# Performance work log

Hardware: AMD Instinct MI355X
Metric: run time of the kernel (lower is better)

## Reference

```python
import jax, jax.numpy as jnp
import numpy as np

EPS = 1e-5
SLOPE = 0.2
K = 20
BINS = [1, 2, 4, 8, 16, 32]


def knn(x_t, k):
    # x_t: (B, N, C) -> idx (B, N, k) of nearest neighbors (by L2, incl. self)
    xx = jnp.sum(x_t * x_t, axis=-1)  # (B, N)
    pd = 2.0 * jnp.einsum('bnc,bmc->bnm', x_t, x_t) - xx[:, :, None] - xx[:, None, :]
    _, idx = jax.lax.top_k(pd, k)
    return idx


def edge_features(x_t, idx):
    # x_t: (B, N, C), idx: (B, N, k) -> (B, N, k, 2C) = [nbr - ctr, ctr]
    B = x_t.shape[0]
    nbr = x_t[jnp.arange(B)[:, None, None], idx]          # (B, N, k, C) gather
    ctr = jnp.broadcast_to(x_t[:, :, None, :], nbr.shape)
    return jnp.concatenate([nbr - ctr, ctr], axis=-1)


def batchnorm(h, gamma, beta, axes):
    # training-mode BN: normalize with batch statistics over `axes` (channel last)
    m = jnp.mean(h, axis=axes, keepdims=True)
    v = jnp.var(h, axis=axes, keepdims=True)
    return (h - m) * jax.lax.rsqrt(v + EPS) * gamma + beta


def lrelu(h):
    return jnp.where(h >= 0, h, SLOPE * h)


def edgeconv(x_t, W, g, b):
    # 1x1 conv over edge features + BN + LeakyReLU + max over k neighbors
    e = edge_features(x_t, knn(x_t, K))            # (B, N, k, 2C)
    h = jnp.einsum('bnkc,oc->bnko', e, W)          # per-edge GEMM
    h = lrelu(batchnorm(h, g, b, (0, 1, 2)))
    return jnp.max(h, axis=2)                      # (B, N, Cout)


def setup_inputs() -> dict:
    key = jax.random.key(0)
    ks = jax.random.split(key, 8)
    B, N = 4, 2048
    d = {'x': jax.random.normal(ks[0], (B, 3, N), dtype=jnp.float32)}
    # conv weights (out, in); BN gamma=1, beta=0 as in torch init
    d['W1'] = jax.random.normal(ks[1], (64, 6), dtype=jnp.float32) * 0.1
    d['g1'] = jnp.ones((64,), jnp.float32); d['b1'] = jnp.zeros((64,), jnp.float32)
    d['W2'] = jax.random.normal(ks[2], (64, 128), dtype=jnp.float32) * 0.1
    d['g2'] = jnp.ones((64,), jnp.float32); d['b2'] = jnp.zeros((64,), jnp.float32)
    d['W3'] = jax.random.normal(ks[3], (128, 128), dtype=jnp.float32) * 0.1
    d['g3'] = jnp.ones((128,), jnp.float32); d['b3'] = jnp.zeros((128,), jnp.float32)
    d['W4'] = jax.random.normal(ks[4], (256, 256), dtype=jnp.float32) * 0.1
    d['g4'] = jnp.ones((256,), jnp.float32); d['b4'] = jnp.zeros((256,), jnp.float32)
    d['W5'] = jax.random.normal(ks[5], (1024, 512), dtype=jnp.float32) * 0.05
    d['g5'] = jnp.ones((1024,), jnp.float32); d['b5'] = jnp.zeros((1024,), jnp.float32)
    d['Wf'] = jax.random.normal(ks[6], (256, 1024), dtype=jnp.float32) * 0.03
    d['bfeat'] = jax.random.normal(ks[7], (256,), dtype=jnp.float32) * 0.01
    return d


def reference(x, W1, g1, b1, W2, g2, b2, W3, g3, b3, W4, g4, b4, W5, g5, b5, Wf, bfeat):
    B, _, N = x.shape
    x_t = jnp.transpose(x, (0, 2, 1))              # (B, N, 3)
    x1 = edgeconv(x_t, W1, g1, b1)                 # (B, N, 64)
    x2 = edgeconv(x1, W2, g2, b2)                  # (B, N, 64)
    x3 = edgeconv(x2, W3, g3, b3)                  # (B, N, 128)
    x4 = edgeconv(x3, W4, g4, b4)                  # (B, N, 256)
    xc = jnp.concatenate([x1, x2, x3, x4], axis=-1)  # (B, N, 512)
    h = jnp.einsum('bnc,oc->bno', xc, W5)          # (B, N, 1024)
    h = lrelu(batchnorm(h, g5, b5, (0, 1)))
    F = h.shape[-1]
    feats = []
    for nb in BINS:  # horizontal pyramid pooling over contiguous point chunks
        z = h.reshape(B, nb, N // nb, F)
        feats.append(jnp.max(z, axis=2) + jnp.mean(z, axis=2))
    bins = jnp.concatenate(feats, axis=1)          # (B, 63, F)
    out = jnp.einsum('bsf,of->sbo', bins, Wf) + bfeat  # (63, B, 256)
    return out
```

## Files before the change

kernel.cpp:

```cpp
#include <hip/hip_runtime.h>
#include <hip/hip_bf16.h>
#include <cstdint>
#include <cstddef>

#define B_SZ   4
#define N_PTS  2048
#define KNN    20
#define BN_ROWS (B_SZ * N_PTS)
#define EPSV   1e-5f
#define SLOPEV 0.2f

typedef __attribute__((ext_vector_type(8))) short bf16x8;
typedef __attribute__((ext_vector_type(4))) float f32x4;

__global__ void k_transpose(const float* __restrict__ x, float* __restrict__ xt,
                            float* __restrict__ xx)
{
    int i = blockIdx.x * 256 + threadIdx.x;
    if (i >= BN_ROWS) return;
    int b = i >> 11, n = i & 2047;
    float v0 = x[((b * 3 + 0) << 11) + n];
    float v1 = x[((b * 3 + 1) << 11) + n];
    float v2 = x[((b * 3 + 2) << 11) + n];
    xt[i * 3 + 0] = v0; xt[i * 3 + 1] = v1; xt[i * 3 + 2] = v2;
    xx[i] = fmaf(v0, v0, fmaf(v1, v1, v2 * v2));
}

__global__ void k_prepw_all(const float* __restrict__ W1, const float* __restrict__ W2,
                            const float* __restrict__ W3, const float* __restrict__ W4,
                            const float* __restrict__ W5, const float* __restrict__ Wf,
                            float* __restrict__ wc, __hip_bfloat16* __restrict__ w5h,
                            float* __restrict__ wft)
{
    int i = blockIdx.x * 256 + threadIdx.x;
    if (i >= 876928) return;
    if (i >= 614784) {
        int e = i - 614784;
        int o = e >> 10, f = e & 1023;
        wft[f * 256 + o] = Wf[e];
        return;
    }
    if (i >= 90496) {
        int e = i - 90496;
        w5h[e] = __float2bfloat16(W5[e]);
        return;
    }
    const float* W; int O, C, off;
    if      (i < 384)   { W = W1; O = 64;  C = 3;   off = 0; }
    else if (i < 8576)  { W = W2; O = 64;  C = 64;  off = 384; }
    else if (i < 24960) { W = W3; O = 128; C = 64;  off = 8576; }
    else                { W = W4; O = 256; C = 128; off = 24960; }
    int e = i - off, j = e / C, c = e - j * C;
    float v;
    if (j < O) v = W[j * 2 * C + c];
    else { int jo = j - O; v = W[jo * 2 * C + C + c] - W[jo * 2 * C + c]; }
    wc[i] = v;
}

template<bool VEC>
__launch_bounds__(512)
__global__ void k_dist(const float* __restrict__ A, int lda,
                       const float* __restrict__ xx,
                       float* __restrict__ C1, int Kd)
{
    constexpr int LDA_ = 132;
    constexpr int LDT_ = 68;
    __shared__ float smem[8704];
    float* As = smem;
    float* Bs = smem + 32 * LDA_;
    float* T  = smem;
    const int tid = threadIdx.x;
    const int tx  = tid & 31;
    const int ty  = tid >> 5;

    int t = blockIdx.x;
    int it, jt;
    if (t < 120) {
        int i = 0;
        for (; i < 15; ++i) { int cnt = 15 - i; if (t < cnt) break; t -= cnt; }
        it = i; jt = i + 1 + t;
    } else {
        it = jt = t - 120;
    }
    const int m0 = it * 128;
    const int n0 = jt * 128;
    const int b  = blockIdx.z;
    const float* Ab = A + (size_t)b * N_PTS * lda;

    float acc[2][4][4] = {};

    for (int k0 = 0; k0 < Kd; k0 += 32) {
        #pragma unroll
        for (int r = 0; r < 2; ++r) {
            int e = r * 512 + tid, row = e >> 3, kq = e & 7;
            if constexpr (VEC) {
                float4 v = *(const float4*)&Ab[(size_t)(m0 + row) * lda + k0 + kq * 4];
                As[(kq * 4 + 0) * LDA_ + row] = v.x;
                As[(kq * 4 + 1) * LDA_ + row] = v.y;
                As[(kq * 4 + 2) * LDA_ + row] = v.z;
                As[(kq * 4 + 3) * LDA_ + row] = v.w;
            } else {
                #pragma unroll
                for (int j = 0; j < 4; ++j) {
                    int kg = k0 + kq * 4 + j;
                    As[(kq * 4 + j) * LDA_ + row] =
                        (kg < Kd) ? Ab[(size_t)(m0 + row) * lda + kg] : 0.f;
                }
            }
        }
        #pragma unroll
        for (int r = 0; r < 2; ++r) {
            int e = r * 512 + tid, row = e >> 3, kq = e & 7;
            if constexpr (VEC) {
                float4 v = *(const float4*)&Ab[(size_t)(n0 + row) * lda + k0 + kq * 4];
                Bs[(kq * 4 + 0) * LDA_ + row] = v.x;
                Bs[(kq * 4 + 1) * LDA_ + row] = v.y;
                Bs[(kq * 4 + 2) * LDA_ + row] = v.z;
                Bs[(kq * 4 + 3) * LDA_ + row] = v.w;
            } else {
                #pragma unroll
                for (int j = 0; j < 4; ++j) {
                    int kg = k0 + kq * 4 + j;
                    Bs[(kq * 4 + j) * LDA_ + row] =
                        (kg < Kd) ? Ab[(size_t)(n0 + row) * lda + kg] : 0.f;
                }
            }
        }
        __syncthreads();

        if constexpr (VEC) {
            float4 ca0 = *(const float4*)&As[ty * 4];
            float4 ca1 = *(const float4*)&As[64 + ty * 4];
            float4 cb  = *(const float4*)&Bs[tx * 4];
            #pragma unroll
            for (int kk = 0; kk < 32; ++kk) {
                float4 na0, na1, nb;
                if (kk < 31) {
                    na0 = *(const float4*)&As[(kk + 1) * LDA_ + ty * 4];
                    na1 = *(const float4*)&As[(kk + 1) * LDA_ + 64 + ty * 4];
                    nb  = *(const float4*)&Bs[(kk + 1) * LDA_ + tx * 4];
                }
                float av[2][4] = {{ca0.x,ca0.y,ca0.z,ca0.w},{ca1.x,ca1.y,ca1.z,ca1.w}};
                float bw[4] = {cb.x, cb.y, cb.z, cb.w};
                #pragma unroll
                for (int ih = 0; ih < 2; ++ih)
                    #pragma unroll
                    for (int ii = 0; ii < 4; ++ii)
                        #pragma unroll
                        for (int jj = 0; jj < 4; ++jj)
                            acc[ih][ii][jj] = fmaf(av[ih][ii], bw[jj], acc[ih][ii][jj]);
                if (kk < 31) { ca0 = na0; ca1 = na1; cb = nb; }
            }
        } else {
            int klen = Kd - k0; if (klen > 32) klen = 32;
            #pragma unroll 8
            for (int kk = 0; kk < klen; ++kk) {
                float4 a0 = *(const float4*)&As[kk * LDA_ + ty * 4];
                float4 a1 = *(const float4*)&As[kk * LDA_ + 64 + ty * 4];
                float4 bq = *(const float4*)&Bs[kk * LDA_ + tx * 4];
                float av[2][4] = {{a0.x,a0.y,a0.z,a0.w},{a1.x,a1.y,a1.z,a1.w}};
                float bw[4] = {bq.x, bq.y, bq.z, bq.w};
                #pragma unroll
                for (int ih = 0; ih < 2; ++ih)
                    #pragma unroll
                    for (int ii = 0; ii < 4; ++ii)
                        #pragma unroll
                        for (int jj = 0; jj < 4; ++jj)
                            acc[ih][ii][jj] = fmaf(av[ih][ii], bw[jj], acc[ih][ii][jj]);
            }
        }
        __syncthreads();
    }

    const float* xxb = xx + b * N_PTS;
    float xj[4];
    {
        float4 v = *(const float4*)&xxb[n0 + tx * 4];
        xj[0] = v.x; xj[1] = v.y; xj[2] = v.z; xj[3] = v.w;
    }
    float xiv[2][4];
    #pragma unroll
    for (int ih = 0; ih < 2; ++ih)
        #pragma unroll
        for (int i = 0; i < 4; ++i)
            xiv[ih][i] = xxb[m0 + ih * 64 + ty * 4 + i];
    const bool diag = (m0 == n0);
    const size_t zoff = (size_t)b * N_PTS;

    #pragma unroll
    for (int ih = 0; ih < 2; ++ih)
        #pragma unroll
        for (int i = 0; i < 4; ++i) {
            int gi = m0 + ih * 64 + ty * 4 + i;
            float xi = xiv[ih][i];
            int gj = n0 + tx * 4;
            float4 v;
            v.x = 2.f * acc[ih][i][0] - xi - xj[0];
            v.y = 2.f * acc[ih][i][1] - xi - xj[1];
            v.z = 2.f * acc[ih][i][2] - xi - xj[2];
            v.w = 2.f * acc[ih][i][3] - xi - xj[3];
            if (diag) {
                if (gi == gj + 0) v.x = 0.f;
                if (gi == gj + 1) v.y = 0.f;
                if (gi == gj + 2) v.z = 0.f;
                if (gi == gj + 3) v.w = 0.f;
            }
            *(float4*)&C1[(zoff + gi) * N_PTS + gj] = v;
        }

    if (!diag) {
        #pragma unroll
        for (int ih = 0; ih < 2; ++ih) {
            #pragma unroll
            for (int c = 0; c < 4; ++c) {
                float xjc = xj[c];
                float4 tv;
                tv.x = 2.f * acc[ih][0][c] - xjc - xiv[ih][0];
                tv.y = 2.f * acc[ih][1][c] - xjc - xiv[ih][1];
                tv.z = 2.f * acc[ih][2][c] - xjc - xiv[ih][2];
                tv.w = 2.f * acc[ih][3][c] - xjc - xiv[ih][3];
                *(float4*)&T[(tx * 4 + c) * LDT_ + ty * 4] = tv;
            }
            __syncthreads();
            #pragma unroll
            for (int r = 0; r < 4; ++r) {
                int e = r * 512 + tid;
                int jr = e >> 4, c4 = e & 15;
                float4 tv = *(const float4*)&T[jr * LDT_ + c4 * 4];
                *(float4*)&C1[(zoff + n0 + jr) * N_PTS + m0 + ih * 64 + c4 * 4] = tv;
            }
            __syncthreads();
        }
    }
}

__launch_bounds__(256)
__global__ void k_gemm5(const unsigned short* __restrict__ Ah,
                        const unsigned short* __restrict__ Bh,
                        float* __restrict__ Cf,
                        float* __restrict__ ssum, float* __restrict__ ssumsq)
{
    constexpr int LDA = 72;
    __shared__ unsigned short As[128 * LDA];
    __shared__ unsigned short Bs[128 * LDA];
    const int tid  = threadIdx.x;
    const int lane = tid & 63;
    const int w    = tid >> 6;
    const int wr   = w >> 1, wcl = w & 1;
    const int quad = lane >> 4;
    const int l16  = lane & 15;
    const int m0 = blockIdx.y * 128;
    const int n0 = blockIdx.x * 128;

    f32x4 acc[4][4] = {};

    for (int k0 = 0; k0 < 512; k0 += 64) {
        #pragma unroll
        for (int r = 0; r < 4; ++r) {
            int e = r * 256 + tid, row = e >> 3, kq = e & 7;
            *(uint4*)&As[row * LDA + kq * 8] =
                *(const uint4*)&Ah[(size_t)(m0 + row) * 512 + k0 + kq * 8];
        }
        #pragma unroll
        for (int r = 0; r < 4; ++r) {
            int e = r * 256 + tid, row = e >> 3, kq = e & 7;
            *(uint4*)&Bs[row * LDA + kq * 8] =
                *(const uint4*)&Bh[(size_t)(n0 + row) * 512 + k0 + kq * 8];
        }
        __syncthreads();
        #pragma unroll
        for (int kk = 0; kk < 64; kk += 32) {
            bf16x8 af[4], bfr[4];
            #pragma unroll
            for (int i = 0; i < 4; ++i)
                af[i] = *(const bf16x8*)&As[(wr * 64 + i * 16 + l16) * LDA + kk + quad * 8];
            #pragma unroll
            for (int j = 0; j < 4; ++j)
                bfr[j] = *(const bf16x8*)&Bs[(wcl * 64 + j * 16 + l16) * LDA + kk + quad * 8];
            #pragma unroll
            for (int i = 0; i < 4; ++i)
                #pragma unroll
                for (int j = 0; j < 4; ++j)
                    acc[i][j] = __builtin_amdgcn_mfma_f32_16x16x32_bf16(af[i], bfr[j], acc[i][j], 0, 0, 0);
        }
        __syncthreads();
    }

    #pragma unroll
    for (int i = 0; i < 4; ++i) {
        int rbase = m0 + wr * 64 + i * 16 + quad * 4;
        #pragma unroll
        for (int j = 0; j < 4; ++j) {
            int col = n0 + wcl * 64 + j * 16 + l16;
            #pragma unroll
            for (int r = 0; r < 4; ++r)
                Cf[(size_t)(rbase + r) * 1024 + col] = acc[i][j][r];
        }
    }

    float* sredS = (float*)As;
    float* sredQ = (float*)Bs;
    #pragma unroll
    for (int j = 0; j < 4; ++j) {
        float s = 0.f, q = 0.f;
        #pragma unroll
        for (int i = 0; i < 4; ++i)
            #pragma unroll
            for (int r = 0; r < 4; ++r) {
                float v = acc[i][j][r];
                s += v; q = fmaf(v, v, q);
            }
        int coll = wcl * 64 + j * 16 + l16;
        int slot = wr * 4 + quad;
        sredS[coll * 8 + slot] = s;
        sredQ[coll * 8 + slot] = q;
    }
    __syncthreads();
    if (tid < 128) {
        float s = 0.f, q = 0.f;
        #pragma unroll
        for (int t = 0; t < 8; ++t) { s += sredS[tid * 8 + t]; q += sredQ[tid * 8 + t]; }
        ssum  [blockIdx.y * 1024 + n0 + tid] = s;
        ssumsq[blockIdx.y * 1024 + n0 + tid] = q;
    }
}

template<bool VEC>
__launch_bounds__(256)
__global__ void k_selgd(const float* __restrict__ D2, int* __restrict__ idx_out,
                        const float* __restrict__ A, int lda,
                        const float* __restrict__ Bm, int ldb,
                        float* __restrict__ C1, float* __restrict__ C2,
                        int Nn, int Kd, int gdBlocks, int gdsh)
{
    constexpr int LDA_ = 132;
    constexpr int LDB_ = 68;
    __shared__ float smem[32 * LDA_ + 32 * LDB_];

    if ((int)blockIdx.x < gdBlocks) {
        float* As = smem;
        float* Bs = smem + 32 * LDA_;
        const int tid = threadIdx.x;
        const int tx  = tid & 15;
        const int ty  = tid >> 4;
        const int gdx = Nn >> 6;
        const int bx  = blockIdx.x & (gdx - 1);
        const int by  = blockIdx.x >> gdsh;
        const int m0 = by * 128;
        const int n0 = bx * 64;

        float acc[2][4][4] = {};

        for (int k0 = 0; k0 < Kd; k0 += 32) {
            #pragma unroll
            for (int r = 0; r < 4; ++r) {
                int e = r * 256 + tid, row = e >> 3, kq = e & 7;
                if constexpr (VEC) {
                    float4 v = *(const float4*)&A[(size_t)(m0 + row) * lda + k0 + kq * 4];
                    As[(kq * 4 + 0) * LDA_ + row] = v.x;
                    As[(kq * 4 + 1) * LDA_ + row] = v.y;
                    As[(kq * 4 + 2) * LDA_ + row] = v.z;
                    As[(kq * 4 + 3) * LDA_ + row] = v.w;
                } else {
                    #pragma unroll
                    for (int j = 0; j < 4; ++j) {
                        int kg = k0 + kq * 4 + j;
                        As[(kq * 4 + j) * LDA_ + row] =
                            (kg < Kd) ? A[(size_t)(m0 + row) * lda + kg] : 0.f;
                    }
                }
            }
            #pragma unroll
            for (int r = 0; r < 2; ++r) {
                int e = r * 256 + tid, row = e >> 3, kq = e & 7;
                if constexpr (VEC) {
                    float4 v = *(const float4*)&Bm[(size_t)(n0 + row) * ldb + k0 + kq * 4];
                    Bs[(kq * 4 + 0) * LDB_ + row] = v.x;
                    Bs[(kq * 4 + 1) * LDB_ + row] = v.y;
                    Bs[(kq * 4 + 2) * LDB_ + row] = v.z;
                    Bs[(kq * 4 + 3) * LDB_ + row] = v.w;
                } else {
                    #pragma unroll
                    for (int j = 0; j < 4; ++j) {
                        int kg = k0 + kq * 4 + j;
                        Bs[(kq * 4 + j) * LDB_ + row] =
                            (kg < Kd) ? Bm[(size_t)(n0 + row) * ldb + kg] : 0.f;
                    }
                }
            }
            __syncthreads();

            if constexpr (VEC) {
                float4 ca0 = *(const float4*)&As[ty * 4];
                float4 ca1 = *(const float4*)&As[64 + ty * 4];
                float4 cb0 = *(const float4*)&Bs[tx * 4];
                #pragma unroll
                for (int kk = 0; kk < 32; ++kk) {
                    float4 na0, na1, nb0;
                    if (kk < 31) {
                        na0 = *(const float4*)&As[(kk + 1) * LDA_ + ty * 4];
                        na1 = *(const float4*)&As[(kk + 1) * LDA_ + 64 + ty * 4];
                        nb0 = *(const float4*)&Bs[(kk + 1) * LDB_ + tx * 4];
                    }
                    float av[2][4] = {{ca0.x,ca0.y,ca0.z,ca0.w},{ca1.x,ca1.y,ca1.z,ca1.w}};
                    float bw[4] = {cb0.x, cb0.y, cb0.z, cb0.w};
                    #pragma unroll
                    for (int ih = 0; ih < 2; ++ih)
                        #pragma unroll
                        for (int ii = 0; ii < 4; ++ii)
                            #pragma unroll
                            for (int jj = 0; jj < 4; ++jj)
                                acc[ih][ii][jj] = fmaf(av[ih][ii], bw[jj], acc[ih][ii][jj]);
                    if (kk < 31) { ca0 = na0; ca1 = na1; cb0 = nb0; }
                }
            } else {
                int klen = Kd - k0; if (klen > 32) klen = 32;
                #pragma unroll 8
                for (int kk = 0; kk < klen; ++kk) {
                    float4 a0 = *(const float4*)&As[kk * LDA_ + ty * 4];
                    float4 a1 = *(const float4*)&As[kk * LDA_ + 64 + ty * 4];
                    float4 bq = *(const float4*)&Bs[kk * LDB_ + tx * 4];
                    float av[2][4] = {{a0.x,a0.y,a0.z,a0.w},{a1.x,a1.y,a1.z,a1.w}};
                    float bw[4] = {bq.x, bq.y, bq.z, bq.w};
                    #pragma unroll
                    for (int ih = 0; ih < 2; ++ih)
                        #pragma unroll
                        for (int ii = 0; ii < 4; ++ii)
                            #pragma unroll
                            for (int jj = 0; jj < 4; ++jj)
                                acc[ih][ii][jj] = fmaf(av[ih][ii], bw[jj], acc[ih][ii][jj]);
                }
            }
            __syncthreads();
        }

        const int Oo = Nn >> 1;
        #pragma unroll
        for (int ih = 0; ih < 2; ++ih)
            #pragma unroll
            for (int i = 0; i < 4; ++i) {
                int row = m0 + ih * 64 + ty * 4 + i;
                int colg = n0 + tx * 4;
                float4 v = make_float4(acc[ih][i][0], acc[ih][i][1],
                                       acc[ih][i][2], acc[ih][i][3]);
                if (colg < Oo) *(float4*)&C1[(size_t)row * Oo + colg] = v;
                else           *(float4*)&C2[(size_t)row * Oo + colg - Oo] = v;
            }
        return;
    }

    const int lane = threadIdx.x & 63;
    const int w    = threadIdx.x >> 6;
    const int qloc = ((int)blockIdx.x - gdBlocks) * 4 + w;
    const float* row = D2 + (size_t)qloc * N_PTS;

    unsigned key[32];
    #pragma unroll
    for (int c = 0; c < 8; ++c) {
        float4 v = *(const float4*)&row[c * 256 + lane * 4];
        float vv[4] = {v.x, v.y, v.z, v.w};
        #pragma unroll
        for (int r = 0; r < 4; ++r) {
            unsigned u = __float_as_uint(vv[r]);
            key[c * 4 + r] = ((int)u >= 0) ? (u | 0x80000000u) : ~u;
        }
    }

    unsigned lmax = 0u;
    #pragma unroll
    for (int e = 0; e < 32; ++e) lmax = (key[e] > lmax) ? key[e] : lmax;
    unsigned gmin = lmax, gmax = lmax;
    #pragma unroll
    for (int s = 32; s >= 1; s >>= 1) {
        unsigned o1 = __shfl_xor(gmin, s, 64);
        unsigned o2 = __shfl_xor(gmax, s, 64);
        gmin = (o1 < gmin) ? o1 : gmin;
        gmax = (o2 > gmax) ? o2 : gmax;
    }

    unsigned lo = gmin, hi2 = gmax;
    while (lo < hi2) {
        unsigned mid = lo + ((hi2 - lo) >> 1);
        int c = __popcll(__ballot(lmax > mid));
        if (c < KNN) hi2 = mid; else lo = mid + 1;
    }
    unsigned hi = gmax;

    unsigned c0 = 0u, c1 = 0u, c2 = 0u, c3 = 0u;
    int nc = 0;
    #pragma unroll
    for (int e = 0; e < 32; ++e) {
        unsigned k = key[e];
        if (k >= lo) {
            if (nc == 0) c0 = k; else if (nc == 1) c1 = k;
            else if (nc == 2) c2 = k; else if (nc == 3) c3 = k;
            ++nc;
        }
    }
    if (__ballot(nc > 4)) {
        while (lo < hi) {
            unsigned mid = lo + ((hi - lo) >> 1);
            int cnt = 0;
            #pragma unroll
            for (int e = 0; e < 32; ++e)
                cnt += __popcll(__ballot(key[e] > mid));
            if (cnt < KNN) hi = mid; else lo = mid + 1;
        }
    } else {
        while (lo < hi) {
            unsigned mid = lo + ((hi - lo) >> 1);
            int cnt = __popcll(__ballot(c0 > mid))
                    + __popcll(__ballot(c1 > mid))
                    + __popcll(__ballot(c2 > mid))
                    + __popcll(__ballot(c3 > mid));
            if (cnt < KNN) hi = mid; else lo = mid + 1;
        }
    }
    const unsigned T = lo;

    int* outp = idx_out + (size_t)qloc * KNN;
    const unsigned long long ltmask = (lane == 0) ? 0ull : (~0ull >> (64 - lane));
    int base = 0;
    #pragma unroll
    for (int e = 0; e < 32; ++e) {
        bool p = key[e] > T;
        unsigned long long m = __ballot(p);
        if (p) {
            int pos = base + __popcll(m & ltmask);
            outp[pos] = (e >> 2) * 256 + lane * 4 + (e & 3);
        }
        base += __popcll(m);
    }
    #pragma unroll
    for (int e = 0; e < 32; ++e) {
        bool p = key[e] == T;
        unsigned long long m = __ballot(p);
        if (p) {
            int pos = base + __popcll(m & ltmask);
            if (pos < KNN) outp[pos] = (e >> 2) * 256 + lane * 4 + (e & 3);
        }
        base += __popcll(m);
    }
}

template<int O, int NSEQ>
__launch_bounds__(256)
__global__ void k_gather(const float* __restrict__ gtab, const float* __restrict__ dtab,
                         const int* __restrict__ idx, const float* __restrict__ gamma,
                         float* __restrict__ hsel,
                         float* __restrict__ ssum, float* __restrict__ ssumsq)
{
    constexpr int NPB = 256 / O;
    const int grp = threadIdx.x / O;
    const int o   = threadIdx.x & (O - 1);
    const float g = gamma[o];
    float accS = 0.f, accS2 = 0.f;
    const int rowsPerBlock = NPB * NSEQ;
    const int batch = blockIdx.x & 3;
    const int chunk = blockIdx.x >> 2;
    const int bbase = batch << 11;
    for (int s = 0; s < NSEQ; ++s) {
        int row = bbase + chunk * rowsPerBlock + s * NPB + grp;
        const int* ip = idx + (size_t)row * KNN;
        float gmax = -INFINITY, gmin = INFINITY, gs = 0.f, gs2 = 0.f;
        for (int k = 0; k < KNN; ++k) {
            int nb = ip[k];
            float v = gtab[(size_t)(bbase + nb) * O + o];
            gmax = fmaxf(gmax, v);
            gmin = fminf(gmin, v);
            gs  += v;
            gs2  = fmaf(v, v, gs2);
        }
        float d = dtab[(size_t)row * O + o];
        float keep = (g >= 0.f) ? gmax : gmin;
        hsel[(size_t)row * O + o] = keep + d;
        accS  += gs + (float)KNN * d;
        accS2 += gs2 + 2.f * d * gs + (float)KNN * d * d;
    }
    int bank = blockIdx.x & 63;
    atomicAdd(&ssum[bank * O + o], accS);
    atomicAdd(&ssumsq[bank * O + o], accS2);
}

template<int O, bool WRITE_XX>
__launch_bounds__(256)
__global__ void k_normalize(const float* __restrict__ hsel,
                            const float* __restrict__ ssum, const float* __restrict__ ssumsq,
                            const float* __restrict__ gamma, const float* __restrict__ beta,
                            float invM, float* __restrict__ xcs,
                            __hip_bfloat16* __restrict__ xch, float* __restrict__ xx)
{
    const int tid = threadIdx.x;
    const int o   = tid & (O - 1);
    float s = 0.f, s2 = 0.f;
    #pragma unroll 8
    for (int bk = 0; bk < 64; ++bk) { s += ssum[bk * O + o]; s2 += ssumsq[bk * O + o]; }
    float mean = s * invM;
    float var  = fmaf(-mean, mean, s2 * invM);
    float sc   = gamma[o] * rsqrtf(var + EPSV);
    float sh   = beta[o] - mean * sc;

    constexpr int R = 256 / O;
    const int rloc = tid / O;
    __shared__ float part[4];
    const int ngroups = BN_ROWS / R;
    for (int gidx = blockIdx.x; gidx < ngroups; gidx += gridDim.x) {
        int row = gidx * R + rloc;
        size_t i = (size_t)row * O + o;
        float h = hsel[i];
        float y = fmaf(h, sc, sh);
        y = (y >= 0.f) ? y : SLOPEV * y;
        xcs[(size_t)row * 512 + o] = y;
        xch[(size_t)row * 512 + o] = __float2bfloat16(y);
        if constexpr (WRITE_XX) {
            float p = y * y;
            #pragma unroll
            for (int sft = 32; sft >= 1; sft >>= 1) p += __shfl_xor(p, sft, 64);
            if constexpr (O == 64) {
                if ((tid & 63) == 0) xx[row] = p;
            } else {
                if ((tid & 63) == 0) part[tid >> 6] = p;
                __syncthreads();
                if constexpr (O == 128) {
                    if (tid < 2) xx[gidx * R + tid] = part[2 * tid] + part[2 * tid + 1];
                } else {
                    if (tid == 0) xx[gidx * R] = (part[0] + part[1]) + (part[2] + part[3]);
                }
                __syncthreads();
            }
        }
    }
}

__global__ void k_seg(const float* __restrict__ h,
                      const float* __restrict__ ssum, const float* __restrict__ ssumsq,
                      const float* __restrict__ gamma, const float* __restrict__ beta,
                      float* __restrict__ smax, float* __restrict__ ssumseg)
{
    int f = blockIdx.y * 256 + threadIdx.x;
    float s = 0.f, s2 = 0.f;
    #pragma unroll 8
    for (int bk = 0; bk < 64; ++bk) { s += ssum[bk * 1024 + f]; s2 += ssumsq[bk * 1024 + f]; }
    const float invM = 1.f / (float)BN_ROWS;
    float mean = s * invM;
    float var  = fmaf(-mean, mean, s2 * invM);
    float sc   = gamma[f] * rsqrtf(var + EPSV);
    float sh   = beta[f] - mean * sc;

    int seg = blockIdx.x;
    float mx = -INFINITY, sm = 0.f;
    int n0 = seg * 64;
    for (int i = 0; i < 64; ++i) {
        float v = fmaf(h[(size_t)(n0 + i) * 1024 + f], sc, sh);
        v = (v >= 0.f) ? v : SLOPEV * v;
        mx = fmaxf(mx, v); sm += v;
    }
    smax[(size_t)seg * 1024 + f]    = mx;
    ssumseg[(size_t)seg * 1024 + f] = sm;
}

__launch_bounds__(256)
__global__ void k_final(const float* __restrict__ smax, const float* __restrict__ ssg,
                        const float* __restrict__ Wft, const float* __restrict__ bfeat,
                        float* __restrict__ out)
{
    __shared__ float row[1024];
    __shared__ float part[1024];
    const int tid = threadIdx.x;
    int sb = blockIdx.x;
    int s = sb >> 2, b = sb & 3;
    int nb = (s == 0) ? 1 : (s < 3) ? 2 : (s < 7) ? 4 : (s < 15) ? 8 : (s < 31) ? 16 : 32;
    int idxL = s - (nb - 1);
    int segc = 32 / nb;
    int seg0 = b * 32 + idxL * segc;
    float inv = 1.f / (float)(64 * segc);
    for (int c = tid; c < 1024; c += 256) {
        float mx = -INFINITY, sm = 0.f;
        for (int t = 0; t < segc; ++t) {
            mx = fmaxf(mx, smax[(size_t)(seg0 + t) * 1024 + c]);
            sm += ssg[(size_t)(seg0 + t) * 1024 + c];
        }
        row[c] = mx + sm * inv;
    }
    __syncthreads();

    const int lane = tid & 63;
    const int w    = tid >> 6;
    const float* rw = row + w * 256;
    const float* wp = Wft + (size_t)(w * 256) * 256 + lane * 4;
    float4 a0 = {0,0,0,0}, a1 = {0,0,0,0}, a2 = {0,0,0,0}, a3 = {0,0,0,0};
    for (int f = 0; f < 256; f += 4) {
        float r0 = rw[f + 0], r1 = rw[f + 1], r2 = rw[f + 2], r3 = rw[f + 3];
        float4 w0 = *(const float4*)&wp[(size_t)(f + 0) * 256];
        float4 w1 = *(const float4*)&wp[(size_t)(f + 1) * 256];
        float4 w2 = *(const float4*)&wp[(size_t)(f + 2) * 256];
        float4 w3 = *(const float4*)&wp[(size_t)(f + 3) * 256];
        a0.x = fmaf(r0, w0.x, a0.x); a0.y = fmaf(r0, w0.y, a0.y);
        a0.z = fmaf(r0, w0.z, a0.z); a0.w = fmaf(r0, w0.w, a0.w);
        a1.x = fmaf(r1, w1.x, a1.x); a1.y = fmaf(r1, w1.y, a1.y);
        a1.z = fmaf(r1, w1.z, a1.z); a1.w = fmaf(r1, w1.w, a1.w);
        a2.x = fmaf(r2, w2.x, a2.x); a2.y = fmaf(r2, w2.y, a2.y);
        a2.z = fmaf(r2, w2.z, a2.z); a2.w = fmaf(r2, w2.w, a2.w);
        a3.x = fmaf(r3, w3.x, a3.x); a3.y = fmaf(r3, w3.y, a3.y);
        a3.z = fmaf(r3, w3.z, a3.z); a3.w = fmaf(r3, w3.w, a3.w);
    }
    float4 a;
    a.x = (a0.x + a1.x) + (a2.x + a3.x);
    a.y = (a0.y + a1.y) + (a2.y + a3.y);
    a.z = (a0.z + a1.z) + (a2.z + a3.z);
    a.w = (a0.w + a1.w) + (a2.w + a3.w);
    *(float4*)&part[w * 256 + lane * 4] = a;
    __syncthreads();
    int o = tid;
    float acc = (part[o] + part[256 + o]) + (part[512 + o] + part[768 + o]);
    out[(size_t)sb * 256 + o] = acc + bfeat[o];
}

extern "C" void kernel_launch(void* const* d_in, const int* in_sizes, int n_in,
                              void* d_out, int out_size, void* d_ws, size_t ws_size,
                              hipStream_t stream)
{
    const float* x  = (const float*)d_in[0];
    const float* W1 = (const float*)d_in[1];
    const float* g1 = (const float*)d_in[2];
    const float* b1 = (const float*)d_in[3];
    const float* W2 = (const float*)d_in[4];
    const float* g2 = (const float*)d_in[5];
    const float* b2 = (const float*)d_in[6];
    const float* W3 = (const float*)d_in[7];
    const float* g3 = (const float*)d_in[8];
    const float* b3 = (const float*)d_in[9];
    const float* W4 = (const float*)d_in[10];
    const float* g4 = (const float*)d_in[11];
    const float* b4 = (const float*)d_in[12];
    const float* W5 = (const float*)d_in[13];
    const float* g5 = (const float*)d_in[14];
    const float* b5 = (const float*)d_in[15];
    const float* Wf = (const float*)d_in[16];
    const float* bfeat = (const float*)d_in[17];
    float* out = (float*)d_out;
    float* ws  = (float*)d_ws;

    float* xt1   = ws + 0;
    int*   idx   = (int*)(ws + 24576);
    float* xx    = ws + 188416;
    float* xc    = ws + 196608;
    float* hsel  = ws + 4390912;
    float* stats = ws + 8585216;
    float* smax  = ws + 8650752;
    float* ssg   = ws + 8781824;
    float* wc    = ws + 8912896;
    float* big   = ws + 9003520;
    __hip_bfloat16* xch = (__hip_bfloat16*)(ws + 25780736);
    __hip_bfloat16* w5h = (__hip_bfloat16*)(ws + 27877888);
    float* wft   = ws + 28140032;
    float* l5s   = ws + 28402176;
    float* l5q   = ws + 28467712;
    float* gtab  = ws + 28533248;
    float* dtab  = ws + 30630400;

    hipMemsetAsync(stats, 0, 65536 * sizeof(float), stream);
    k_transpose<<<32, 256, 0, stream>>>(x, xt1, xx);
    k_prepw_all<<<3426, 256, 0, stream>>>(W1, W2, W3, W4, W5, Wf, wc, w5h, wft);

    const float invMk = 1.f / (float)(BN_ROWS * KNN);

    {
        float* ss = stats + 0;
        k_dist<false><<<dim3(136, 1, 4), 512, 0, stream>>>(xt1, 3, xx, big, 3);
        k_selgd<false><<<128 + 2048, 256, 0, stream>>>(big, idx, xt1, 3, wc, 3, gtab, dtab, 128, 3, 128, 1);
        k_gather<64, 8><<<256, 256, 0, stream>>>(gtab, dtab, idx, g1, hsel, ss, ss + 4096);
        k_normalize<64, true><<<512, 256, 0, stream>>>(hsel, ss, ss + 4096, g1, b1, invMk, xc + 0, xch + 0, xx);
    }
    {
        float* ss = stats + 8192;
        k_dist<true><<<dim3(136, 1, 4), 512, 0, stream>>>(xc + 0, 512, xx, big, 64);
        k_selgd<true><<<128 + 2048, 256, 0, stream>>>(big, idx, xc + 0, 512, wc + 384, 64, gtab, dtab, 128, 64, 128, 1);
        k_gather<64, 8><<<256, 256, 0, stream>>>(gtab, dtab, idx, g2, hsel, ss, ss + 4096);
        k_normalize<64, true><<<512, 256, 0, stream>>>(hsel, ss, ss + 4096, g2, b2, invMk, xc + 64, xch + 64, xx);
    }
    {
        float* ss = stats + 16384;
        k_dist<true><<<dim3(136, 1, 4), 512, 0, stream>>>(xc + 64, 512, xx, big, 64);
        k_selgd<true><<<256 + 2048, 256, 0, stream>>>(big, idx, xc + 64, 512, wc + 8576, 64, gtab, dtab, 256, 64, 256, 2);
        k_gather<128, 8><<<512, 256, 0, stream>>>(gtab, dtab, idx, g3, hsel, ss, ss + 8192);
        k_normalize<128, true><<<512, 256, 0, stream>>>(hsel, ss, ss + 8192, g3, b3, invMk, xc + 128, xch + 128, xx);
    }
    {
        float* ss = stats + 32768;
        k_dist<true><<<dim3(136, 1, 4), 512, 0, stream>>>(xc + 128, 512, xx, big, 128);
        k_selgd<true><<<512 + 2048, 256, 0, stream>>>(big, idx, xc + 128, 512, wc + 24960, 128, gtab, dtab, 512, 128, 512, 3);
        k_gather<256, 8><<<1024, 256, 0, stream>>>(gtab, dtab, idx, g4, hsel, ss, ss + 16384);
        k_normalize<256, false><<<512, 256, 0, stream>>>(hsel, ss, ss + 16384, g4, b4, invMk, xc + 256, xch + 256, xx);
    }
    {
        k_gemm5<<<dim3(8, 64), 256, 0, stream>>>((const unsigned short*)xch, (const unsigned short*)w5h, big, l5s, l5q);
        k_seg<<<dim3(128, 4), 256, 0, stream>>>(big, l5s, l5q, g5, b5, smax, ssg);
        k_final<<<252, 256, 0, stream>>>(smax, ssg, wft, bfeat, out);
    }
}
```

Measured before the change: 488.2 us.

## Double-buffer shared-memory tiles in vectorized pairwise-distance GEMM kernel

Restructures the VEC path of the k_dist distance GEMM to use two shared-memory stages. The global loads for the next K-slice are issued into registers before the current slice's FMA loop and stored into the alternate buffer afterwards, so each step needs one barrier instead of two. Shared memory per block roughly doubles (about 34 KB to about 68 KB), which may reduce occupancy. The non-vectorized path is unchanged apart from being split out.

```diff
diff --git a/kernel.cpp b/kernel.cpp
--- a/kernel.cpp
+++ b/kernel.cpp
@@ -65,9 +65,8 @@
 {
     constexpr int LDA_ = 132;
     constexpr int LDT_ = 68;
-    __shared__ float smem[8704];
-    float* As = smem;
-    float* Bs = smem + 32 * LDA_;
+    constexpr int BUFF = 32 * LDA_ * 2;
+    __shared__ float smem[2 * BUFF];
     float* T  = smem;
     const int tid = threadIdx.x;
     const int tx  = tid & 31;
@@ -89,56 +88,67 @@
 
     float acc[2][4][4] = {};
 
-    for (int k0 = 0; k0 < Kd; k0 += 32) {
-        #pragma unroll
-        for (int r = 0; r < 2; ++r) {
-            int e = r * 512 + tid, row = e >> 3, kq = e & 7;
-            if constexpr (VEC) {
-                float4 v = *(const float4*)&Ab[(size_t)(m0 + row) * lda + k0 + kq * 4];
-                As[(kq * 4 + 0) * LDA_ + row] = v.x;
-                As[(kq * 4 + 1) * LDA_ + row] = v.y;
-                As[(kq * 4 + 2) * LDA_ + row] = v.z;
-                As[(kq * 4 + 3) * LDA_ + row] = v.w;
-            } else {
-                #pragma unroll
-                for (int j = 0; j < 4; ++j) {
-                    int kg = k0 + kq * 4 + j;
-                    As[(kq * 4 + j) * LDA_ + row] =
-                        (kg < Kd) ? Ab[(size_t)(m0 + row) * lda + kg] : 0.f;
-                }
-            }
-        }
-        #pragma unroll
-        for (int r = 0; r < 2; ++r) {
-            int e = r * 512 + tid, row = e >> 3, kq = e & 7;
-            if constexpr (VEC) {
-                float4 v = *(const float4*)&Ab[(size_t)(n0 + row) * lda + k0 + kq * 4];
-                Bs[(kq * 4 + 0) * LDA_ + row] = v.x;
-                Bs[(kq * 4 + 1) * LDA_ + row] = v.y;
-                Bs[(kq * 4 + 2) * LDA_ + row] = v.z;
-                Bs[(kq * 4 + 3) * LDA_ + row] = v.w;
-            } else {
-                #pragma unroll
-                for (int j = 0; j < 4; ++j) {
-                    int kg = k0 + kq * 4 + j;
-                    Bs[(kq * 4 + j) * LDA_ + row] =
-                        (kg < Kd) ? Ab[(size_t)(n0 + row) * lda + kg] : 0.f;
-                }
-            }
-        }
+    if constexpr (VEC) {
+        const int nst  = Kd >> 5;
+        const int row0 = tid >> 3, kq0 = tid & 7;
+        const float* gA0 = Ab + (size_t)(m0 + row0) * lda + kq0 * 4;
+        const float* gA1 = Ab + (size_t)(m0 + row0 + 64) * lda + kq0 * 4;
+        const float* gB0 = Ab + (size_t)(n0 + row0) * lda + kq0 * 4;
+        const float* gB1 = Ab + (size_t)(n0 + row0 + 64) * lda + kq0 * 4;
+        const int s0 = (kq0 * 4) * LDA_ + row0;
+
+        float4 pA0, pA1, pB0, pB1;
+
+#define KD_STORE_TILE(BASEPTR) do {                                  \
+        float* As_m = (BASEPTR);                                     \
+        float* Bs_m = (BASEPTR) + 32 * LDA_;                         \
+        As_m[s0 + 0 * LDA_]      = pA0.x;                            \
+        As_m[s0 + 1 * LDA_]      = pA0.y;                            \
+        As_m[s0 + 2 * LDA_]      = pA0.z;                            \
+        As_m[s0 + 3 * LDA_]      = pA0.w;                            \
+        As_m[s0 + 0 * LDA_ + 64] = pA1.x;                            \
+        As_m[s0 + 1 * LDA_ + 64] = pA1.y;                            \
+        As_m[s0 + 2 * LDA_ + 64] = pA1.z;                            \
+        As_m[s0 + 3 * LDA_ + 64] = pA1.w;                            \
+        Bs_m[s0 + 0 * LDA_]      = pB0.x;                            \
+        Bs_m[s0 + 1 * LDA_]      = pB0.y;                            \
+        Bs_m[s0 + 2 * LDA_]      = pB0.z;                            \
+        Bs_m[s0 + 3 * LDA_]      = pB0.w;                            \
+        Bs_m[s0 + 0 * LDA_ + 64] = pB1.x;                            \
+        Bs_m[s0 + 1 * LDA_ + 64] = pB1.y;                            \
+        Bs_m[s0 + 2 * LDA_ + 64] = pB1.z;                            \
+        Bs_m[s0 + 3 * LDA_ + 64] = pB1.w;                            \
+    } while (0)
+
+        pA0 = *(const float4*)(gA0);
+        pA1 = *(const float4*)(gA1);
+        pB0 = *(const float4*)(gB0);
+        pB1 = *(const float4*)(gB1);
+        KD_STORE_TILE(smem);
         __syncthreads();
 
-        if constexpr (VEC) {
-            float4 ca0 = *(const float4*)&As[ty * 4];
-            float4 ca1 = *(const float4*)&As[64 + ty * 4];
-            float4 cb  = *(const float4*)&Bs[tx * 4];
+        for (int step = 0; step < nst; ++step) {
+            float* As_ = smem + (step & 1) * BUFF;
+            float* Bs_ = As_ + 32 * LDA_;
+            const bool more = (step + 1 < nst);
+            if (more) {
+                const int ko = (step + 1) << 5;
+                pA0 = *(const float4*)(gA0 + ko);
+                pA1 = *(const float4*)(gA1 + ko);
+                pB0 = *(const float4*)(gB0 + ko);
+                pB1 = *(const float4*)(gB1 + ko);
+            }
+
+            float4 ca0 = *(const float4*)&As_[ty * 4];
+            float4 ca1 = *(const float4*)&As_[64 + ty * 4];
+            float4 cb  = *(const float4*)&Bs_[tx * 4];
             #pragma unroll
             for (int kk = 0; kk < 32; ++kk) {
                 float4 na0, na1, nb;
                 if (kk < 31) {
-                    na0 = *(const float4*)&As[(kk + 1) * LDA_ + ty * 4];
-                    na1 = *(const float4*)&As[(kk + 1) * LDA_ + 64 + ty * 4];
-                    nb  = *(const float4*)&Bs[(kk + 1) * LDA_ + tx * 4];
+                    na0 = *(const float4*)&As_[(kk + 1) * LDA_ + ty * 4];
+                    na1 = *(const float4*)&As_[(kk + 1) * LDA_ + 64 + ty * 4];
+                    nb  = *(const float4*)&Bs_[(kk + 1) * LDA_ + tx * 4];
                 }
                 float av[2][4] = {{ca0.x,ca0.y,ca0.z,ca0.w},{ca1.x,ca1.y,ca1.z,ca1.w}};
                 float bw[4] = {cb.x, cb.y, cb.z, cb.w};
@@ -151,7 +161,36 @@
                             acc[ih][ii][jj] = fmaf(av[ih][ii], bw[jj], acc[ih][ii][jj]);
                 if (kk < 31) { ca0 = na0; ca1 = na1; cb = nb; }
             }
-        } else {
+            if (more) KD_STORE_TILE(smem + ((step + 1) & 1) * BUFF);
+            __syncthreads();
+        }
+#undef KD_STORE_TILE
+    } else {
+        float* As = smem;
+        float* Bs = smem + 32 * LDA_;
+        for (int k0 = 0; k0 < Kd; k0 += 32) {
+            #pragma unroll
+            for (int r = 0; r < 2; ++r) {
+                int e = r * 512 + tid, row = e >> 3, kq = e & 7;
+                #pragma unroll
+                for (int j = 0; j < 4; ++j) {
+                    int kg = k0 + kq * 4 + j;
+                    As[(kq * 4 + j) * LDA_ + row] =
+                        (kg < Kd) ? Ab[(size_t)(m0 + row) * lda + kg] : 0.f;
+                }
+            }
+            #pragma unroll
+            for (int r = 0; r < 2; ++r) {
+                int e = r * 512 + tid, row = e >> 3, kq = e & 7;
+                #pragma unroll
+                for (int j = 0; j < 4; ++j) {
+                    int kg = k0 + kq * 4 + j;
+                    Bs[(kq * 4 + j) * LDA_ + row] =
+                        (kg < Kd) ? Ab[(size_t)(n0 + row) * lda + kg] : 0.f;
+                }
+            }
+            __syncthreads();
+
             int klen = Kd - k0; if (klen > 32) klen = 32;
             #pragma unroll 8
             for (int kk = 0; kk < klen; ++kk) {
@@ -168,8 +207,8 @@
                         for (int jj = 0; jj < 4; ++jj)
                             acc[ih][ii][jj] = fmaf(av[ih][ii], bw[jj], acc[ih][ii][jj]);
             }
-        }
-        __syncthreads();
+            __syncthreads();
+        }
     }
 
     const float* xxb = xx + b * N_PTS;
```

Result: slower. 1.109 ms (+127.1%).
